# Kernel tuning notes

Measured on AMD Instinct MI355X. Metric: run time of the kernel, lower is better.

The kernel has to match this reference:

```python
import jax, jax.numpy as jnp
import numpy as np

NUM_NODES, NODE_F = 50000, 128
NUM_EDGES, EDGE_F = 500000, 128
B, N = 4096, 100
D = 64      # node_dim
T = 8       # time_dim
LN_EPS = 1e-5


def setup_inputs() -> dict:
    key = jax.random.key(0)
    ks = jax.random.split(key, 16)
    inp = {
        'src_neighbor_node_ids': jax.random.randint(ks[0], (B, N), 0, NUM_NODES),
        'src_neighbor_edge_ids': jax.random.randint(ks[1], (B, N), 0, NUM_EDGES),
        'src_neighbor_times': jax.random.uniform(ks[2], (B, N), dtype=jnp.float32),
        'dst_node_ids': jax.random.randint(ks[3], (B,), 0, NUM_NODES),
        'node_raw_features': jax.random.normal(ks[4], (NUM_NODES, NODE_F), jnp.float32),
        'edge_raw_features': jax.random.normal(ks[5], (NUM_EDGES, EDGE_F), jnp.float32),
        # projection layers (stored as [in, out])
        'W_feat': jax.random.normal(ks[6], (NODE_F, D), jnp.float32) / np.sqrt(NODE_F),
        'b_feat': jnp.zeros((D,), jnp.float32),
        'W_edge': jax.random.normal(ks[7], (1, D), jnp.float32),
        'b_edge': jnp.zeros((D,), jnp.float32),
        'W_time': jax.random.normal(ks[8], (T, D), jnp.float32) / np.sqrt(T),
        'b_time': jnp.zeros((D,), jnp.float32),
        'W_struct': jax.random.normal(ks[9], (1, D), jnp.float32),
        'b_struct': jnp.zeros((D,), jnp.float32),
        # time encoder (cosine basis with log-spaced frequencies)
        'w_tenc': (1.0 / 10 ** np.linspace(0, 9, T)).astype(np.float32),
        'b_tenc': jnp.zeros((T,), jnp.float32),
        # layernorm
        'ln_g': jnp.ones((D,), jnp.float32),
        'ln_b': jnp.zeros((D,), jnp.float32),
        # GCNConv
        'W_gcn': jax.random.normal(ks[10], (D, D), jnp.float32) / np.sqrt(D),
        'b_gcn': jnp.zeros((D,), jnp.float32),
        # output layer
        'W_out': jax.random.normal(ks[11], (D, D), jnp.float32) / np.sqrt(D),
        'b_out': jnp.zeros((D,), jnp.float32),
    }
    return inp


def reference(src_neighbor_node_ids, src_neighbor_edge_ids, src_neighbor_times,
              dst_node_ids, node_raw_features, edge_raw_features,
              W_feat, b_feat, W_edge, b_edge, W_time, b_time, W_struct, b_struct,
              w_tenc, b_tenc, ln_g, ln_b, W_gcn, b_gcn, W_out, b_out):
    f32 = jnp.float32
    nbr_raw = node_raw_features[src_neighbor_node_ids]            # [B,N,F]
    node_f = nbr_raw @ W_feat + b_feat                            # [B,N,D]
    edge_col = edge_raw_features[src_neighbor_edge_ids, 0][..., None]  # [B,N,1]
    edge_f = edge_col @ W_edge + b_edge
    t_enc = jnp.cos(src_neighbor_times[..., None] * w_tenc + b_tenc)   # [B,N,T]
    time_f = t_enc @ W_time + b_time
    co = (src_neighbor_node_ids == dst_node_ids[:, None]).astype(f32)[..., None]
    co_f = co @ W_struct + b_struct
    skill_nbr = nbr_raw[..., 0].astype(jnp.int32)                 # [B,N]
    skill_dst = node_raw_features[dst_node_ids, 0].astype(jnp.int32)  # [B]
    sim = (skill_nbr == skill_dst[:, None]).astype(f32)[..., None]
    sim_f = sim @ W_struct + b_struct
    fused = node_f + edge_f + time_f + co_f + sim_f               # [B,N,D]
    mu = fused.mean(-1, keepdims=True)
    var = ((fused - mu) ** 2).mean(-1, keepdims=True)
    fused = (fused - mu) * jax.lax.rsqrt(var + LN_EPS) * ln_g + ln_b
    # per-sample chain GCN: directed edges j -> j+1 for j in [0, v-2], v = #valid ids,
    # PyG gcn_norm with self loops: deg[j] = 1 + in_degree[j]
    h = fused @ W_gcn                                             # [B,N,D]
    v = (src_neighbor_node_ids > 0).sum(-1)                       # [B]
    pos = jnp.arange(N)[None, :]                                  # [1,N]
    has_in = ((pos >= 1) & (pos < v[:, None])).astype(f32)        # [B,N]
    deg = 1.0 + has_in
    dinv_sqrt = jax.lax.rsqrt(deg)
    h_prev = jnp.pad(h[:, :-1], ((0, 0), (1, 0), (0, 0)))
    d_prev = jnp.pad(dinv_sqrt[:, :-1], ((0, 0), (1, 0)))
    out = h / deg[..., None] + (has_in * d_prev * dinv_sqrt)[..., None] * h_prev + b_gcn
    gnn = jax.nn.relu(out)
    src_emb = gnn.mean(axis=1)                                    # [B,D] global_mean_pool over N
    dst_emb = node_raw_features[dst_node_ids] @ W_feat + b_feat
    src_emb = src_emb @ W_out + b_out
    dst_emb = dst_emb @ W_out + b_out
    return src_emb, dst_emb
```

## Files before the change

kernel.cpp:

```cpp
#include <hip/hip_runtime.h>
#include <stdint.h>

#define NUM_NODES 50000
#define NUM_EDGES 500000
#define B_ 4096
#define N_ 100

typedef float f32x4 __attribute__((ext_vector_type(4)));
typedef float f32x2 __attribute__((ext_vector_type(2)));
typedef int   i32x4 __attribute__((ext_vector_type(4)));
typedef short s16x8 __attribute__((ext_vector_type(8)));

__device__ inline unsigned short f2bf(float f) {
    unsigned u = __float_as_uint(f);
    u += 0x7fffu + ((u >> 16) & 1u);
    return (unsigned short)(u >> 16);
}

template <int CTRL>
__device__ inline float dpp_add(float x) {
    int t = __builtin_amdgcn_update_dpp(0, __float_as_int(x), CTRL, 0xf, 0xf, true);
    return x + __int_as_float(t);
}
__device__ inline float wave_sum64(float x) {
    x = dpp_add<0x111>(x);
    x = dpp_add<0x112>(x);
    x = dpp_add<0x114>(x);
    x = dpp_add<0x118>(x);
    x = dpp_add<0x142>(x);
    x = dpp_add<0x143>(x);
    return __int_as_float(__builtin_amdgcn_readlane(__float_as_int(x), 63));
}

__global__ __launch_bounds__(256) void k_edge(
    const float* __restrict__ edge_raw, float* __restrict__ edge0)
{
    int i = blockIdx.x * 256 + threadIdx.x;
    int stride = gridDim.x * 256;
    for (; i < NUM_EDGES; i += stride)
        edge0[i] = edge_raw[(size_t)i * 128];
}

__global__ __launch_bounds__(256) void k_pre(
    const float* __restrict__ node_raw, const float* __restrict__ W_feat,
    const float* __restrict__ b_feat, const float* __restrict__ W_gcn,
    const float* __restrict__ ln_g, const float* __restrict__ ln_b,
    const float* __restrict__ W_edge, const float* __restrict__ b_edge,
    const float* __restrict__ W_time, const float* __restrict__ b_time,
    const float* __restrict__ W_struct, const float* __restrict__ b_struct,
    float* __restrict__ proj, int* __restrict__ skill,
    float* __restrict__ hb, float* __restrict__ wmg, float* __restrict__ Mg,
    unsigned short* __restrict__ PGmF)
{
    __shared__ float red[4][64];
    __shared__ float PGms[12][64];
    __shared__ unsigned short WfB[16][64][8];
    int blk = blockIdx.x;
    int t = threadIdx.x;
    int dj = t & 63;

    if (blk == gridDim.x - 1) {
        int g = t >> 6;
        float acc = 0.f;
        #pragma unroll
        for (int i = 0; i < 16; ++i) {
            int dk = g * 16 + i;
            acc += ln_b[dk] * W_gcn[dk * 64 + dj];
        }
        red[g][dj] = acc;

        if (t < 64) {
            int d = t;
            float col[11];
            col[0] = W_edge[d];
            col[1] = W_struct[d];
            #pragma unroll
            for (int i = 0; i < 8; ++i) col[2 + i] = W_time[i * 64 + d];
            col[10] = b_edge[d] + b_time[d] + 2.f * b_struct[d];
            float wmv[11];
            #pragma unroll
            for (int j = 0; j < 11; ++j) wmv[j] = wave_sum64(col[j]) * (1.f / 64.f);
            float cc[11];
            #pragma unroll
            for (int j = 0; j < 11; ++j) cc[j] = col[j] - wmv[j];
            #pragma unroll
            for (int j = 0; j < 11; ++j) {
                #pragma unroll
                for (int k = j; k < 11; ++k) {
                    float m = wave_sum64(cc[j] * cc[k]);
                    if (t == 0) { Mg[j * 11 + k] = m; Mg[k * 11 + j] = m; }
                }
            }
            if (t == 0) {
                #pragma unroll
                for (int j = 0; j < 11; ++j) wmg[j] = wmv[j];
            }

            int j = t;
            float accp[12];
            #pragma unroll
            for (int m = 0; m < 12; ++m) accp[m] = 0.f;
            for (int d2 = 0; d2 < 64; ++d2) {
                float gg = ln_g[d2] * W_gcn[d2 * 64 + j];
                float bias_d = b_edge[d2] + b_time[d2] + 2.f * b_struct[d2];
                accp[0] = fmaf(W_edge[d2], gg, accp[0]);
                accp[1] = fmaf(W_struct[d2], gg, accp[1]);
                #pragma unroll
                for (int i = 0; i < 8; ++i)
                    accp[2 + i] = fmaf(W_time[i * 64 + d2], gg, accp[2 + i]);
                accp[10] = fmaf(bias_d, gg, accp[10]);
                accp[11] += gg;
            }
            #pragma unroll
            for (int m = 0; m < 12; ++m) PGms[m][j] = accp[m];
        }
        __syncthreads();
        if (g == 0) hb[dj] = red[0][dj] + red[1][dj] + red[2][dj] + red[3][dj];

        {
            int ct = t >> 6, l = t & 63;
            int col = ct * 16 + (l & 15);
            int ks = (l >> 4) * 8;
            s16x8 a2;
            #pragma unroll
            for (int j2 = 0; j2 < 8; ++j2) {
                int k = ks + j2;
                a2[j2] = (k < 12) ? (short)f2bf(PGms[k][col]) : (short)0;
            }
            *(s16x8*)(PGmF + ((size_t)ct * 64 + l) * 8) = a2;
        }
        return;
    }

    #pragma unroll
    for (int i = 0; i < 4; ++i) {
        int e = t + i * 256;
        int tile = e >> 6;
        int l = e & 63;
        int ct = tile >> 2, kt = tile & 3;
        int col = ct * 16 + (l & 15);
        int ks = kt * 32 + (l >> 4) * 8;
        s16x8 a;
        #pragma unroll
        for (int j = 0; j < 8; ++j)
            a[j] = (short)f2bf(W_feat[(ks + j) * 64 + col]);
        *(s16x8*)&WfB[tile][l][0] = a;
    }
    __syncthreads();

    int w = t >> 6, lane = t & 63;
    int rbase = blk * 64 + w * 16;
    int rA = rbase + (lane & 15);
    int rc = rA < NUM_NODES ? rA : (NUM_NODES - 1);
    int kq = lane >> 4;

    s16x8 A[4];
    float a0x = 0.f;
    #pragma unroll
    for (int kt = 0; kt < 4; ++kt) {
        const float* src = node_raw + (size_t)rc * 128 + kt * 32 + kq * 8;
        f32x4 v0 = *(const f32x4*)src;
        f32x4 v1 = *(const f32x4*)(src + 4);
        s16x8 a;
        a[0] = (short)f2bf(v0.x); a[1] = (short)f2bf(v0.y);
        a[2] = (short)f2bf(v0.z); a[3] = (short)f2bf(v0.w);
        a[4] = (short)f2bf(v1.x); a[5] = (short)f2bf(v1.y);
        a[6] = (short)f2bf(v1.z); a[7] = (short)f2bf(v1.w);
        A[kt] = a;
        if (kt == 0) a0x = v0.x;
    }
    if (kq == 0 && rA < NUM_NODES) skill[rA] = (int)a0x;

    f32x4 acc[4];
    #pragma unroll
    for (int ct = 0; ct < 4; ++ct) { f32x4 z = {0.f,0.f,0.f,0.f}; acc[ct] = z; }
    #pragma unroll
    for (int ct = 0; ct < 4; ++ct) {
        #pragma unroll
        for (int kt = 0; kt < 4; ++kt) {
            s16x8 bfr = *(const s16x8*)&WfB[ct * 4 + kt][lane][0];
            acc[ct] = __builtin_amdgcn_mfma_f32_16x16x32_bf16(A[kt], bfr, acc[ct], 0, 0, 0);
        }
    }
    #pragma unroll
    for (int ct = 0; ct < 4; ++ct) {
        int col = ct * 16 + (lane & 15);
        float bf = b_feat[col];
        #pragma unroll
        for (int j = 0; j < 4; ++j) {
            int row = rbase + kq * 4 + j;
            if (row < NUM_NODES)
                proj[(size_t)row * 64 + col] = acc[ct][j] + bf;
        }
    }
}

__global__ __launch_bounds__(256) void k_pg(
    const float* __restrict__ proj, const float* __restrict__ W_gcn,
    const float* __restrict__ ln_g,
    const float* __restrict__ W_out, const float* __restrict__ b_out,
    const float* __restrict__ W_edge, const float* __restrict__ b_edge,
    const float* __restrict__ W_time, const float* __restrict__ b_time,
    const float* __restrict__ W_struct, const float* __restrict__ b_struct,
    float* __restrict__ projG, float* __restrict__ dstE,
    float* __restrict__ stats)
{
    __shared__ unsigned short WgB[8][64][8];
    __shared__ unsigned short WoB[8][64][8];
    __shared__ unsigned short WsB[2][64][8];
    int t = threadIdx.x;

    #pragma unroll
    for (int i = 0; i < 2; ++i) {
        int e = t + i * 256;
        int tile = e >> 6, l = e & 63;
        int ct = tile >> 1, kt = tile & 1;
        int col = ct * 16 + (l & 15);
        int ks = kt * 32 + (l >> 4) * 8;
        s16x8 a, b2;
        #pragma unroll
        for (int j = 0; j < 8; ++j) {
            int k = ks + j;
            a[j]  = (short)f2bf(ln_g[k] * W_gcn[k * 64 + col]);
            b2[j] = (short)f2bf(W_out[k * 64 + col]);
        }
        *(s16x8*)&WgB[tile][l][0] = a;
        *(s16x8*)&WoB[tile][l][0] = b2;
    }
    if (t < 128) {
        int kt = t >> 6, l = t & 63;
        int col = l & 15;
        int ks = kt * 32 + (l >> 4) * 8;
        s16x8 a;
        #pragma unroll
        for (int j = 0; j < 8; ++j) {
            int d = ks + j;
            float v;
            if (col == 0) v = W_edge[d];
            else if (col == 1) v = W_struct[d];
            else if (col < 10) v = W_time[(col - 2) * 64 + d];
            else if (col == 10) v = b_edge[d] + b_time[d] + 2.f * b_struct[d];
            else if (col == 11) v = 1.f;
            else v = 0.f;
            a[j] = (short)f2bf(v);
        }
        *(s16x8*)&WsB[kt][l][0] = a;
    }
    __syncthreads();

    int w = t >> 6, lane = t & 63;
    int rbase = blockIdx.x * 64 + w * 16;
    int rA = rbase + (lane & 15);
    int rc = rA < NUM_NODES ? rA : (NUM_NODES - 1);
    int kq = lane >> 4;

    s16x8 Ahi[2], Alo[2], Qhi[2], Qlo[2];
    #pragma unroll
    for (int kt = 0; kt < 2; ++kt) {
        const float* src = proj + (size_t)rc * 64 + kt * 32 + kq * 8;
        f32x4 v0 = *(const f32x4*)src;
        f32x4 v1 = *(const f32x4*)(src + 4);
        #pragma unroll
        for (int j = 0; j < 8; ++j) {
            float v = (j < 4) ? v0[j] : v1[j - 4];
            unsigned short hi = f2bf(v);
            float rem = v - __uint_as_float((unsigned)hi << 16);
            Ahi[kt][j] = (short)hi;
            Alo[kt][j] = (short)f2bf(rem);
            float p2 = v * v;
            unsigned short h2 = f2bf(p2);
            float r2 = p2 - __uint_as_float((unsigned)h2 << 16);
            Qhi[kt][j] = (short)h2;
            Qlo[kt][j] = (short)f2bf(r2);
        }
    }

    f32x4 accG[4], accE[4];
    f32x4 accS = {0.f, 0.f, 0.f, 0.f}, accQ = {0.f, 0.f, 0.f, 0.f};
    #pragma unroll
    for (int ct = 0; ct < 4; ++ct) {
        f32x4 z = {0.f, 0.f, 0.f, 0.f};
        accG[ct] = z; accE[ct] = z;
    }
    #pragma unroll
    for (int ct = 0; ct < 4; ++ct) {
        #pragma unroll
        for (int kt = 0; kt < 2; ++kt) {
            s16x8 bg = *(const s16x8*)&WgB[ct * 2 + kt][lane][0];
            accG[ct] = __builtin_amdgcn_mfma_f32_16x16x32_bf16(Alo[kt], bg, accG[ct], 0, 0, 0);
            accG[ct] = __builtin_amdgcn_mfma_f32_16x16x32_bf16(Ahi[kt], bg, accG[ct], 0, 0, 0);
            s16x8 bo = *(const s16x8*)&WoB[ct * 2 + kt][lane][0];
            accE[ct] = __builtin_amdgcn_mfma_f32_16x16x32_bf16(Alo[kt], bo, accE[ct], 0, 0, 0);
            accE[ct] = __builtin_amdgcn_mfma_f32_16x16x32_bf16(Ahi[kt], bo, accE[ct], 0, 0, 0);
        }
    }
    #pragma unroll
    for (int kt = 0; kt < 2; ++kt) {
        s16x8 bs = *(const s16x8*)&WsB[kt][lane][0];
        accS = __builtin_amdgcn_mfma_f32_16x16x32_bf16(Alo[kt], bs, accS, 0, 0, 0);
        accS = __builtin_amdgcn_mfma_f32_16x16x32_bf16(Ahi[kt], bs, accS, 0, 0, 0);
        accQ = __builtin_amdgcn_mfma_f32_16x16x32_bf16(Qlo[kt], bs, accQ, 0, 0, 0);
        accQ = __builtin_amdgcn_mfma_f32_16x16x32_bf16(Qhi[kt], bs, accQ, 0, 0, 0);
    }

    #pragma unroll
    for (int ct = 0; ct < 4; ++ct) {
        int col = ct * 16 + (lane & 15);
        float bo_ = b_out[col];
        #pragma unroll
        for (int j = 0; j < 4; ++j) {
            int row = rbase + kq * 4 + j;
            if (row < NUM_NODES) {
                projG[(size_t)row * 64 + col] = accG[ct][j];
                dstE[(size_t)row * 64 + col] = accE[ct][j] + bo_;
            }
        }
    }
    int c = lane & 15;
    if (c <= 11) {
        #pragma unroll
        for (int j = 0; j < 4; ++j) {
            int row = rbase + kq * 4 + j;
            if (row < NUM_NODES) stats[(size_t)row * 16 + c] = accS[j];
        }
    }
    if (c == 11) {
        #pragma unroll
        for (int j = 0; j < 4; ++j) {
            int row = rbase + kq * 4 + j;
            if (row < NUM_NODES) stats[(size_t)row * 16 + 12] = accQ[j];
        }
    }
}

__global__ __launch_bounds__(256) void k_main(
    const int* __restrict__ ids, const int* __restrict__ eids,
    const float* __restrict__ times, const int* __restrict__ dst_ids,
    const float* __restrict__ edge0,
    const float* __restrict__ w_tenc, const float* __restrict__ b_tenc,
    const float* __restrict__ b_gcn, const float* __restrict__ W_out,
    const float* __restrict__ b_out,
    const float* __restrict__ projG, const float* __restrict__ dstE,
    const int* __restrict__ skill,
    const float* __restrict__ hb, const float* __restrict__ wmg,
    const float* __restrict__ Mg, const unsigned short* __restrict__ PGmF,
    const float* __restrict__ stats,
    float* __restrict__ out)
{
    __shared__ int ids_s[112];
    __shared__ unsigned short VA[112 * 32];
    __shared__ float rstd_s[112];
    __shared__ f32x2 cf_s[112];
    __shared__ float pooled[64];
    __shared__ int vcnt_w[4];

    int b = blockIdx.x;
    int t = threadIdx.x;
    int lane = t & 63, w = t >> 6;

    int dstb = dst_ids[b];
    int skdst = skill[dstb];

    int idx_c = t < N_ ? t : 0;
    int id_t = ids[b * N_ + idx_c];
    float tm_t = times[b * N_ + idx_c];
    int ei_t = eids[b * N_ + idx_c];
    float e_t = edge0[ei_t];
    int sk_t = skill[id_t];
    const f32x4* sp4 = (const f32x4*)(stats + (size_t)id_t * 16);
    f32x4 s0 = sp4[0], s1 = sp4[1], s2 = sp4[2], s3 = sp4[3];

    if (t < 112) ids_s[t] = (t < N_) ? id_t : 0;
    unsigned long long bal = __ballot((t < N_) && (id_t > 0));
    if (lane == 0) vcnt_w[w] = __popcll(bal);
    float tc[8];
    #pragma unroll
    for (int i = 0; i < 8; ++i) tc[i] = __cosf(fmaf(tm_t, w_tenc[i], b_tenc[i]));
    __syncthreads();
    int v = vcnt_w[0] + vcnt_w[1] + vcnt_w[2] + vcnt_w[3];

    int colw = 16 * w + (lane & 15);
    int kq = lane >> 4;
    float pgv[7][4];
    #pragma unroll
    for (int mt = 0; mt < 7; ++mt) {
        i32x4 s4 = *(const i32x4*)&ids_s[mt * 16 + kq * 4];
        #pragma unroll
        for (int j = 0; j < 4; ++j)
            pgv[mt][j] = projG[(size_t)s4[j] * 64 + colw];
    }
    if (w == 3)
        out[(size_t)(B_ + b) * 64 + lane] = dstE[(size_t)dstb * 64 + lane];

    if (t < 112) {
        int n = t;
        bool hin = (n >= 1) && (n < v);
        float a_ = hin ? 0.5f : 1.f;
        float dprev = (n >= 2 && n <= v) ? 0.70710678118f : 1.f;
        float coef = hin ? dprev * 0.70710678118f : 0.f;
        f32x2 cf = {a_, coef};
        cf_s[t] = cf;
    }

    if (t < N_) {
        float u[11];
        u[0] = e_t;
        u[1] = (id_t == dstb ? 1.f : 0.f) + (sk_t == skdst ? 1.f : 0.f);
        #pragma unroll
        for (int i = 0; i < 8; ++i) u[2 + i] = tc[i];
        u[10] = 1.f;

        float pwv[11] = {s0.x, s0.y, s0.z, s0.w, s1.x, s1.y, s1.z, s1.w,
                         s2.x, s2.y, s2.z};
        float sp = s2.w;
        float spp = s3.x;
        float dot_upw = 0.f, su_wm = 0.f;
        #pragma unroll
        for (int j = 0; j < 11; ++j) {
            dot_upw = fmaf(u[j], pwv[j], dot_upw);
            su_wm = fmaf(u[j], wmg[j], su_wm);
        }
        float mu = sp * (1.f / 64.f) + su_wm;
        float q = spp + sp * sp * (1.f / 64.f) + 2.f * dot_upw - 2.f * sp * mu;
        #pragma unroll
        for (int j = 0; j < 11; ++j) {
            float tj = 0.f;
            #pragma unroll
            for (int k = 0; k < 11; ++k) tj = fmaf(Mg[j * 11 + k], u[k], tj);
            q = fmaf(u[j], tj, q);
        }
        float rstd = rsqrtf(fmaxf(q, 0.f) * (1.f / 64.f) + 1e-5f);
        rstd_s[t] = rstd;

        unsigned short vv[32];
        #pragma unroll
        for (int j = 0; j < 11; ++j) vv[j] = f2bf(rstd * u[j]);
        vv[11] = f2bf(-rstd * mu);
        #pragma unroll
        for (int j = 12; j < 32; ++j) vv[j] = 0;
        #pragma unroll
        for (int c = 0; c < 4; ++c)
            *(s16x8*)((char*)VA + t * 64 + ((c ^ (t & 3)) * 16)) = *(const s16x8*)&vv[c * 8];
    } else if (t < 112) {
        rstd_s[t] = 0.f;
        s16x8 z = {0, 0, 0, 0, 0, 0, 0, 0};
        #pragma unroll
        for (int c = 0; c < 4; ++c)
            *(s16x8*)((char*)VA + t * 64 + c * 16) = z;
    }
    __syncthreads();

    s16x8 bfr = *(const s16x8*)(PGmF + ((size_t)w * 64 + lane) * 8);
    f32x4 acc[7];
    #pragma unroll
    for (int mt = 0; mt < 7; ++mt) {
        int row = mt * 16 + (lane & 15);
        s16x8 a = *(const s16x8*)((char*)VA + row * 64 + ((kq ^ (row & 3)) * 16));
        f32x4 z = {0.f, 0.f, 0.f, 0.f};
        acc[mt] = __builtin_amdgcn_mfma_f32_16x16x32_bf16(a, bfr, z, 0, 0, 0);
    }

    float hbv = hb[colw], bgc = b_gcn[colw];
    float carry = 0.f, po = 0.f;
    #pragma unroll
    for (int mt = 0; mt < 7; ++mt) {
        int nb = mt * 16 + kq * 4;
        f32x4 rs4 = *(const f32x4*)&rstd_s[nb];
        f32x4 cf01 = *(const f32x4*)&cf_s[nb];
        f32x4 cf23 = *(const f32x4*)&cf_s[nb + 2];
        float hh[4];
        #pragma unroll
        for (int j = 0; j < 4; ++j)
            hh[j] = fmaf(rs4[j], pgv[mt][j], acc[mt][j]) + hbv;

        float hup = __shfl_up(hh[3], 16, 64);
        float hpj = (kq > 0) ? hup : carry;

        float o0 = fmaf(hh[0], cf01.x, fmaf(cf01.y, hpj, bgc));
        float o1 = fmaf(hh[1], cf01.z, fmaf(cf01.w, hh[0], bgc));
        float o2 = fmaf(hh[2], cf23.x, fmaf(cf23.y, hh[1], bgc));
        float o3 = fmaf(hh[3], cf23.z, fmaf(cf23.w, hh[2], bgc));
        if (nb < N_)     po += fmaxf(o0, 0.f);
        if (nb + 1 < N_) po += fmaxf(o1, 0.f);
        if (nb + 2 < N_) po += fmaxf(o2, 0.f);
        if (nb + 3 < N_) po += fmaxf(o3, 0.f);

        carry = __shfl(hh[3], 48 + (lane & 15), 64);
    }
    po += __shfl_xor(po, 16, 64);
    po += __shfl_xor(po, 32, 64);
    if (lane < 16) pooled[colw] = po * (1.f / (float)N_);
    __syncthreads();

    if (w == 0) {
        float o = b_out[lane];
        #pragma unroll
        for (int dk4 = 0; dk4 < 16; ++dk4) {
            f32x4 p4 = *(const f32x4*)&pooled[dk4 * 4];
            o = fmaf(p4.x, W_out[(dk4 * 4 + 0) * 64 + lane], o);
            o = fmaf(p4.y, W_out[(dk4 * 4 + 1) * 64 + lane], o);
            o = fmaf(p4.z, W_out[(dk4 * 4 + 2) * 64 + lane], o);
            o = fmaf(p4.w, W_out[(dk4 * 4 + 3) * 64 + lane], o);
        }
        out[(size_t)b * 64 + lane] = o;
    }
}

extern "C" void kernel_launch(void* const* d_in, const int* in_sizes, int n_in,
                              void* d_out, int out_size, void* d_ws, size_t ws_size,
                              hipStream_t stream)
{
    const int*   ids      = (const int*)d_in[0];
    const int*   eids     = (const int*)d_in[1];
    const float* times    = (const float*)d_in[2];
    const int*   dst_ids  = (const int*)d_in[3];
    const float* node_raw = (const float*)d_in[4];
    const float* edge_raw = (const float*)d_in[5];
    const float* W_feat   = (const float*)d_in[6];
    const float* b_feat   = (const float*)d_in[7];
    const float* W_edge   = (const float*)d_in[8];
    const float* b_edge   = (const float*)d_in[9];
    const float* W_time   = (const float*)d_in[10];
    const float* b_time   = (const float*)d_in[11];
    const float* W_struct = (const float*)d_in[12];
    const float* b_struct = (const float*)d_in[13];
    const float* w_tenc   = (const float*)d_in[14];
    const float* b_tenc   = (const float*)d_in[15];
    const float* ln_g     = (const float*)d_in[16];
    const float* ln_b     = (const float*)d_in[17];
    const float* W_gcn    = (const float*)d_in[18];
    const float* b_gcn    = (const float*)d_in[19];
    const float* W_out    = (const float*)d_in[20];
    const float* b_out    = (const float*)d_in[21];

    char* ws = (char*)d_ws;
    float*          proj   = (float*)ws;
    int*            skill  = (int*)(ws + 12800000);
    float*          hb     = (float*)(ws + 13008192);
    float*          wmg    = (float*)(ws + 13008448);
    float*          Mg     = (float*)(ws + 13008512);
    unsigned short* PGmF   = (unsigned short*)(ws + 13009024);
    float*          stats  = (float*)(ws + 13100032);
    float*          projG  = (float*)(ws + 16400000);
    float*          dstE   = (float*)(ws + 29200000);
    float*          edge0  = (float*)(ws + 42000000);

    k_edge<<<1024, 256, 0, stream>>>(edge_raw, edge0);
    k_pre<<<783, 256, 0, stream>>>(node_raw, W_feat, b_feat, W_gcn, ln_g, ln_b,
                                   W_edge, b_edge, W_time, b_time, W_struct, b_struct,
                                   proj, skill, hb, wmg, Mg, PGmF);
    k_pg<<<782, 256, 0, stream>>>(proj, W_gcn, ln_g, W_out, b_out,
                                  W_edge, b_edge, W_time, b_time, W_struct, b_struct,
                                  projG, dstE, stats);
    k_main<<<B_, 256, 0, stream>>>(ids, eids, times, dst_ids, edge0,
                                   w_tenc, b_tenc, b_gcn, W_out, b_out,
                                   projG, dstE, skill, hb, wmg, Mg, PGmF, stats,
                                   (float*)d_out);
}
```

Baseline: 80.15 us.

## Store projG as bf16, fold edge extraction into k_pre, cache skill in stats

Stores the per-node GCN projection as bf16 instead of fp32, halving the bytes k_main gathers for each neighbor. Merges the separate edge-column extraction kernel into k_pre as extra blocks, which removes a launch and lets that work overlap with the node projection. Writes each node's skill value into a spare slot of the stats row, so k_main reads it with the stats it already loads instead of doing a separate gather. The bf16 storage lowers the precision of the GCN input.

```diff
diff --git a/kernel.cpp b/kernel.cpp
--- a/kernel.cpp
+++ b/kernel.cpp
@@ -32,15 +32,6 @@
     return __int_as_float(__builtin_amdgcn_readlane(__float_as_int(x), 63));
 }
 
-__global__ __launch_bounds__(256) void k_edge(
-    const float* __restrict__ edge_raw, float* __restrict__ edge0)
-{
-    int i = blockIdx.x * 256 + threadIdx.x;
-    int stride = gridDim.x * 256;
-    for (; i < NUM_EDGES; i += stride)
-        edge0[i] = edge_raw[(size_t)i * 128];
-}
-
 __global__ __launch_bounds__(256) void k_pre(
     const float* __restrict__ node_raw, const float* __restrict__ W_feat,
     const float* __restrict__ b_feat, const float* __restrict__ W_gcn,
@@ -48,9 +39,10 @@
     const float* __restrict__ W_edge, const float* __restrict__ b_edge,
     const float* __restrict__ W_time, const float* __restrict__ b_time,
     const float* __restrict__ W_struct, const float* __restrict__ b_struct,
+    const float* __restrict__ edge_raw,
     float* __restrict__ proj, int* __restrict__ skill,
     float* __restrict__ hb, float* __restrict__ wmg, float* __restrict__ Mg,
-    unsigned short* __restrict__ PGmF)
+    unsigned short* __restrict__ PGmF, float* __restrict__ edge0)
 {
     __shared__ float red[4][64];
     __shared__ float PGms[12][64];
@@ -132,6 +124,15 @@
         return;
     }
 
+    if (blk >= 782) {
+        int base = (blk - 782) * 512;
+        int e0 = base + t;
+        if (e0 < NUM_EDGES) edge0[e0] = edge_raw[(size_t)e0 * 128];
+        int e1 = base + 256 + t;
+        if (e1 < NUM_EDGES) edge0[e1] = edge_raw[(size_t)e1 * 128];
+        return;
+    }
+
     #pragma unroll
     for (int i = 0; i < 4; ++i) {
         int e = t + i * 256;
@@ -202,7 +203,8 @@
     const float* __restrict__ W_edge, const float* __restrict__ b_edge,
     const float* __restrict__ W_time, const float* __restrict__ b_time,
     const float* __restrict__ W_struct, const float* __restrict__ b_struct,
-    float* __restrict__ projG, float* __restrict__ dstE,
+    const int* __restrict__ skill,
+    unsigned short* __restrict__ projGh, float* __restrict__ dstE,
     float* __restrict__ stats)
 {
     __shared__ unsigned short WgB[8][64][8];
@@ -311,7 +313,7 @@
         for (int j = 0; j < 4; ++j) {
             int row = rbase + kq * 4 + j;
             if (row < NUM_NODES) {
-                projG[(size_t)row * 64 + col] = accG[ct][j];
+                projGh[(size_t)row * 64 + col] = f2bf(accG[ct][j]);
                 dstE[(size_t)row * 64 + col] = accE[ct][j] + bo_;
             }
         }
@@ -329,6 +331,13 @@
         for (int j = 0; j < 4; ++j) {
             int row = rbase + kq * 4 + j;
             if (row < NUM_NODES) stats[(size_t)row * 16 + 12] = accQ[j];
+        }
+    }
+    if (c == 12) {
+        #pragma unroll
+        for (int j = 0; j < 4; ++j) {
+            int row = rbase + kq * 4 + j;
+            if (row < NUM_NODES) stats[(size_t)row * 16 + 13] = (float)skill[row];
         }
     }
 }
@@ -340,8 +349,7 @@
     const float* __restrict__ w_tenc, const float* __restrict__ b_tenc,
     const float* __restrict__ b_gcn, const float* __restrict__ W_out,
     const float* __restrict__ b_out,
-    const float* __restrict__ projG, const float* __restrict__ dstE,
-    const int* __restrict__ skill,
+    const unsigned short* __restrict__ projGh, const float* __restrict__ dstE,
     const float* __restrict__ hb, const float* __restrict__ wmg,
     const float* __restrict__ Mg, const unsigned short* __restrict__ PGmF,
     const float* __restrict__ stats,
@@ -359,14 +367,13 @@
     int lane = t & 63, w = t >> 6;
 
     int dstb = dst_ids[b];
-    int skdst = skill[dstb];
+    float skdstf = stats[(size_t)dstb * 16 + 13];
 
     int idx_c = t < N_ ? t : 0;
     int id_t = ids[b * N_ + idx_c];
     float tm_t = times[b * N_ + idx_c];
     int ei_t = eids[b * N_ + idx_c];
     float e_t = edge0[ei_t];
-    int sk_t = skill[id_t];
     const f32x4* sp4 = (const f32x4*)(stats + (size_t)id_t * 16);
     f32x4 s0 = sp4[0], s1 = sp4[1], s2 = sp4[2], s3 = sp4[3];
 
@@ -386,8 +393,10 @@
     for (int mt = 0; mt < 7; ++mt) {
         i32x4 s4 = *(const i32x4*)&ids_s[mt * 16 + kq * 4];
         #pragma unroll
-        for (int j = 0; j < 4; ++j)
-            pgv[mt][j] = projG[(size_t)s4[j] * 64 + colw];
+        for (int j = 0; j < 4; ++j) {
+            unsigned short pv = projGh[(size_t)s4[j] * 64 + colw];
+            pgv[mt][j] = __uint_as_float((unsigned)pv << 16);
+        }
     }
     if (w == 3)
         out[(size_t)(B_ + b) * 64 + lane] = dstE[(size_t)dstb * 64 + lane];
@@ -405,7 +414,7 @@
     if (t < N_) {
         float u[11];
         u[0] = e_t;
-        u[1] = (id_t == dstb ? 1.f : 0.f) + (sk_t == skdst ? 1.f : 0.f);
+        u[1] = (id_t == dstb ? 1.f : 0.f) + (s3.y == skdstf ? 1.f : 0.f);
         #pragma unroll
         for (int i = 0; i < 8; ++i) u[2 + i] = tc[i];
         u[10] = 1.f;
@@ -541,19 +550,18 @@
     float*          Mg     = (float*)(ws + 13008512);
     unsigned short* PGmF   = (unsigned short*)(ws + 13009024);
     float*          stats  = (float*)(ws + 13100032);
-    float*          projG  = (float*)(ws + 16400000);
+    unsigned short* projGh = (unsigned short*)(ws + 16400000);
     float*          dstE   = (float*)(ws + 29200000);
     float*          edge0  = (float*)(ws + 42000000);
 
-    k_edge<<<1024, 256, 0, stream>>>(edge_raw, edge0);
-    k_pre<<<783, 256, 0, stream>>>(node_raw, W_feat, b_feat, W_gcn, ln_g, ln_b,
-                                   W_edge, b_edge, W_time, b_time, W_struct, b_struct,
-                                   proj, skill, hb, wmg, Mg, PGmF);
+    k_pre<<<1760, 256, 0, stream>>>(node_raw, W_feat, b_feat, W_gcn, ln_g, ln_b,
+                                    W_edge, b_edge, W_time, b_time, W_struct, b_struct,
+                                    edge_raw, proj, skill, hb, wmg, Mg, PGmF, edge0);
     k_pg<<<782, 256, 0, stream>>>(proj, W_gcn, ln_g, W_out, b_out,
                                   W_edge, b_edge, W_time, b_time, W_struct, b_struct,
-                                  projG, dstE, stats);
+                                  skill, projGh, dstE, stats);
     k_main<<<B_, 256, 0, stream>>>(ids, eids, times, dst_ids, edge0,
                                    w_tenc, b_tenc, b_gcn, W_out, b_out,
-                                   projG, dstE, skill, hb, wmg, Mg, PGmF, stats,
+                                   projGh, dstE, hb, wmg, Mg, PGmF, stats,
                                    (float*)d_out);
 }
```

Measured after the change: 73.45 us. 1.09x faster.
